# Optimization experiments

Measured on AMD Instinct MI355X. Metric: run time of the kernel, lower is better.

The kernel has to match this reference:

```python
import jax, jax.numpy as jnp
import numpy as np

N, E, C, H = 50000, 800000, 64, 64  # nodes, edges, channels, mlp hidden


def _seg_softmax(logits, seg, num_segments):
    # per-destination-node, per-channel softmax over incoming edges (PyG softmax)
    m = jax.ops.segment_max(logits, seg, num_segments=num_segments)
    m = jnp.where(jnp.isfinite(m), m, 0.0)
    e = jnp.exp(logits - m[seg])
    s = jax.ops.segment_sum(e, seg, num_segments=num_segments)
    return e / (s[seg] + 1e-16)


def setup_inputs() -> dict:
    key = jax.random.key(0)
    ks = jax.random.split(key, 16)

    def w(k, shape, fan_in):
        lim = 1.0 / np.sqrt(fan_in)
        return jax.random.uniform(k, shape, jnp.float32, -lim, lim)

    return dict(
        x=jax.random.normal(ks[0], (N, C), jnp.float32),
        pos=jax.random.uniform(ks[1], (N, 3), jnp.float32),
        edge_index=jax.random.randint(ks[2], (2, E), 0, N),
        # lin_in (Linear with bias)
        W_in=w(ks[3], (C, C), C), b_in=jnp.zeros((C,), jnp.float32),
        # PointTransformerConv internal linears (bias=False in PyG)
        W_lin=w(ks[4], (C, C), C),
        W_src=w(ks[5], (C, C), C),
        W_dst=w(ks[6], (C, C), C),
        # pos_nn: Linear(3,64) + ReLU + Linear(64,C)
        Wp1=w(ks[7], (3, H), 3), bp1=jnp.zeros((H,), jnp.float32),
        Wp2=w(ks[8], (H, C), H), bp2=jnp.zeros((C,), jnp.float32),
        # attn_nn: Linear(C,64) + ReLU + Linear(64,C)
        Wa1=w(ks[9], (C, H), C), ba1=jnp.zeros((H,), jnp.float32),
        Wa2=w(ks[10], (H, C), H), ba2=jnp.zeros((C,), jnp.float32),
        # lin_out
        W_out=w(ks[11], (C, C), C), b_out=jnp.zeros((C,), jnp.float32),
    )


def reference(x, pos, edge_index, W_in, b_in, W_lin, W_src, W_dst,
              Wp1, bp1, Wp2, bp2, Wa1, ba1, Wa2, ba2, W_out, b_out):
    n = x.shape[0]
    src, dst = edge_index[0], edge_index[1]
    # lin_in + ReLU
    h = jax.nn.relu(x @ W_in + b_in)                      # [N,C]
    # PointTransformerConv projections
    v = h @ W_lin                                         # values [N,C]
    a_src = h @ W_src                                     # alpha_j source term
    a_dst = h @ W_dst                                     # alpha_i dest term
    # per-edge positional encoding: pos_nn(pos_i - pos_j)
    rel = pos[dst] - pos[src]                             # [E,3]
    delta = jax.nn.relu(rel @ Wp1 + bp1) @ Wp2 + bp2      # [E,C]
    # attention logits: attn_nn(alpha_i - alpha_j + delta)
    alpha = a_dst[dst] - a_src[src] + delta               # [E,C]
    alpha = jax.nn.relu(alpha @ Wa1 + ba1) @ Wa2 + ba2    # [E,C]
    alpha = _seg_softmax(alpha, dst, n)
    # weighted scatter-sum aggregation: sum_j alpha * (x_j + delta)
    out = jax.ops.segment_sum(alpha * (v[src] + delta), dst, num_segments=n)
    # lin_out + ReLU
    return jax.nn.relu(out @ W_out + b_out)
```

## Files before the change

### kernel.cpp

```cpp
#include <hip/hip_runtime.h>

typedef unsigned short u16;
typedef unsigned int   u32;
typedef unsigned long long u64;
typedef __attribute__((ext_vector_type(8))) short bf16x8;
typedef __attribute__((ext_vector_type(4))) float f32x4;

#define DEV static __device__ __forceinline__

DEV u16 f2bf(float f){ union{float f; u32 i;} v; v.f=f; u32 u=v.i;
                       return (u16)((u + 0x7FFFu + ((u>>16)&1u))>>16); }
DEV float bf2f(u16 u){ union{u32 i; float f;} v; v.i=((u32)u)<<16; return v.f; }
DEV float bfl(u32 w){ return bf2f((u16)(w & 0xffffu)); }
DEV float bfh(u32 w){ return bf2f((u16)(w >> 16)); }
DEV u32 pk2(float a, float b){ return (u32)f2bf(a) | ((u32)f2bf(b) << 16); }
DEV void ldsfence(){ asm volatile("s_waitcnt lgkmcnt(0)" ::: "memory"); }

#define NBIAS 384
#define FB_P1 0
#define FB_P2 4
#define FB_A1 12
#define FB_A2 20
#define FB_IN 28
#define FB_LIN 36
#define FB_SRC 44
#define FB_DST 52
#define FB_OUT 60
#define NFRAG 68

#define LROW 70
#define LROWD 35

DEV bf16x8 fb_load(const u16* __restrict__ FB, int frag, int lane){
  union{ uint4 u; bf16x8 v; } w;
  w.u = *(const uint4*)(FB + ((size_t)(frag*64+lane))*8);
  return w.v;
}
DEV bf16x8 lds_read_chunk(const u32* l32, int dw){
  union{ u32 d[4]; bf16x8 v; } u;
#pragma unroll
  for(int p=0;p<4;p++) u.d[p] = l32[dw+p];
  return u.v;
}

__global__ __launch_bounds__(256) void k_prep(
  const float* __restrict__ Win, const float* __restrict__ Wlin,
  const float* __restrict__ Wsrc, const float* __restrict__ Wdst,
  const float* __restrict__ Wp1, const float* __restrict__ Wp2,
  const float* __restrict__ Wa1, const float* __restrict__ Wa2,
  const float* __restrict__ Wout,
  const float* __restrict__ bin, const float* __restrict__ bp1, const float* __restrict__ bp2,
  const float* __restrict__ ba1, const float* __restrict__ ba2, const float* __restrict__ bout,
  float* __restrict__ Bf, u16* __restrict__ FB)
{
  int idx = blockIdx.x*256 + threadIdx.x;
  if(idx < NBIAS){
    int which = idx >> 6, c = idx & 63;
    if(which == 3){
      float sacc = ba1[c];
      for(int k=0;k<64;k++) sacc += bp2[k]*Wa1[k*64+c];
      Bf[idx] = sacc;
    } else {
      const float* b;
      switch(which){ case 0:b=bin;break; case 1:b=bp1;break; case 2:b=bp2;break;
                     case 4:b=ba2;break; default:b=bout;break; }
      Bf[idx] = b[c];
    }
  } else if(idx < NBIAS + NFRAG*64){
    int j = idx - NBIAS;
    int frag = j >> 6, lane = j & 63;
    int t = lane & 15, q = lane >> 4;
    const float* src = nullptr; const float* fuse = nullptr;
    int K = 64, nt, s;
    if(frag < 4){ src = Wp1; K = 3; nt = frag; s = 0; }
    else if(frag < 12){ int g=frag-4;  src=Wp2;  nt=g>>1; s=g&1; }
    else if(frag < 20){ int g=frag-12; fuse=Wp2; nt=g>>1; s=g&1; }
    else if(frag < 28){ int g=frag-20; src=Wa2;  nt=g>>1; s=g&1; }
    else if(frag < 36){ int g=frag-28; src=Win;  nt=g>>1; s=g&1; }
    else if(frag < 44){ int g=frag-36; src=Wlin; nt=g>>1; s=g&1; }
    else if(frag < 52){ int g=frag-44; fuse=Wsrc; nt=g>>1; s=g&1; }
    else if(frag < 60){ int g=frag-52; fuse=Wdst; nt=g>>1; s=g&1; }
    else              { int g=frag-60; src=Wout; nt=g>>1; s=g&1; }
    u16* dst = FB + ((size_t)(frag*64+lane))*8;
    if(fuse){
      int col = nt*16 + t;
#pragma unroll
      for(int jj=0;jj<8;jj++){
        int k = s*32 + q*8 + jj;
        const float* ar = fuse + k*64;
        float accv = 0.f;
        for(int m=0;m<64;m++) accv += ar[m] * Wa1[m*64+col];
        dst[jj] = f2bf(accv);
      }
    } else {
#pragma unroll
      for(int jj=0;jj<8;jj++){
        int k = s*32 + q*8 + jj;
        dst[jj] = (k<K) ? f2bf(src[k*64 + nt*16 + t]) : (u16)0;
      }
    }
  }
}

__global__ __launch_bounds__(256) void k_node_m(
  const float* __restrict__ x, const float* __restrict__ Bf, const u16* __restrict__ FB,
  u16* __restrict__ vf, u16* __restrict__ asof, u16* __restrict__ adof,
  int N, int ntiles)
{
  __shared__ u16 sc16[4][16*LROW];
  int lane = threadIdx.x & 63, warp = threadIdx.x >> 6;
  int t = lane & 15, q = lane >> 4;
  int tile = blockIdx.x*4 + warp;
  if(tile >= ntiles) return;
  u16* lb = sc16[warp]; u32* lb32 = (u32*)lb;
  int r0 = tile*16;
  int row = r0 + t; if(row >= N) row = N-1;

  const float4* x4 = (const float4*)(x + (size_t)row*64);
  bf16x8 xa[2];
#pragma unroll
  for(int s=0;s<2;s++){
    float4 u0 = x4[s*8 + q*2], u1 = x4[s*8 + q*2 + 1];
    xa[s][0]=(short)f2bf(u0.x); xa[s][1]=(short)f2bf(u0.y);
    xa[s][2]=(short)f2bf(u0.z); xa[s][3]=(short)f2bf(u0.w);
    xa[s][4]=(short)f2bf(u1.x); xa[s][5]=(short)f2bf(u1.y);
    xa[s][6]=(short)f2bf(u1.z); xa[s][7]=(short)f2bf(u1.w);
  }
  f32x4 zero = {0.f,0.f,0.f,0.f};
  f32x4 acc[4];
#pragma unroll
  for(int nt=0;nt<4;nt++){
    acc[nt] = __builtin_amdgcn_mfma_f32_16x16x32_bf16(xa[0], fb_load(FB, FB_IN+nt*2+0, lane), zero, 0,0,0);
    acc[nt] = __builtin_amdgcn_mfma_f32_16x16x32_bf16(xa[1], fb_load(FB, FB_IN+nt*2+1, lane), acc[nt], 0,0,0);
  }
#pragma unroll
  for(int nt=0;nt<4;nt++)
#pragma unroll
    for(int r=0;r<4;r++)
      lb[(q*4+r)*LROW + nt*16 + t] = f2bf(fmaxf(acc[nt][r] + Bf[nt*16+t], 0.f));
  ldsfence();
  bf16x8 h0 = lds_read_chunk(lb32, t*LROWD + q*4);
  bf16x8 h1 = lds_read_chunk(lb32, t*LROWD + 16 + q*4);

  const int fb0[3] = {FB_LIN, FB_SRC, FB_DST};
  u16* Os[3] = {vf, asof, adof};
#pragma unroll
  for(int mtx=0; mtx<3; mtx++){
    f32x4 av[4];
#pragma unroll
    for(int nt=0;nt<4;nt++){
      av[nt] = __builtin_amdgcn_mfma_f32_16x16x32_bf16(h0, fb_load(FB, fb0[mtx]+nt*2+0, lane), zero, 0,0,0);
      av[nt] = __builtin_amdgcn_mfma_f32_16x16x32_bf16(h1, fb_load(FB, fb0[mtx]+nt*2+1, lane), av[nt], 0,0,0);
    }
    u16* O = Os[mtx];
#pragma unroll
    for(int r=0;r<4;r++){
      int rr = r0 + q*4 + r;
      if(rr < N){
        uint2 o;
        o.x = (u32)f2bf(av[0][r]) | ((u32)f2bf(av[1][r]) << 16);
        o.y = (u32)f2bf(av[2][r]) | ((u32)f2bf(av[3][r]) << 16);
        *(uint2*)(O + (size_t)rr*64 + t*4) = o;
      }
    }
  }
}

__global__ __launch_bounds__(256) void k_hist(const int* __restrict__ ei, int* __restrict__ deg, int E){
  int e = blockIdx.x*256 + threadIdx.x;
  if(e < E) atomicAdd(&deg[ei[(size_t)E + e]], 1);
}

__global__ __launch_bounds__(256) void k_scanA(const int* __restrict__ deg,
    int* __restrict__ row_start, int* __restrict__ bsum, int N){
  __shared__ int b[256];
  int tid = threadIdx.x, i = blockIdx.x*256 + tid;
  int v = (i<N) ? deg[i] : 0;
  b[tid] = v; __syncthreads();
#pragma unroll
  for(int off=1; off<256; off<<=1){
    int u = (tid>=off) ? b[tid-off] : 0;
    __syncthreads(); b[tid] += u; __syncthreads();
  }
  if(i<N) row_start[i] = b[tid] - v;
  if(tid==255) bsum[blockIdx.x] = b[255];
}
__global__ __launch_bounds__(256) void k_scanB(int* __restrict__ bsum,
    int* __restrict__ bsoff, int* __restrict__ row_start, int nb, int N){
  __shared__ int b[256];
  int tid = threadIdx.x;
  int v = (tid<nb) ? bsum[tid] : 0;
  b[tid] = v; __syncthreads();
#pragma unroll
  for(int off=1; off<256; off<<=1){
    int u = (tid>=off) ? b[tid-off] : 0;
    __syncthreads(); b[tid] += u; __syncthreads();
  }
  if(tid<nb) bsoff[tid] = b[tid] - v;
  if(tid==255) row_start[N] = b[255];
}
__global__ __launch_bounds__(256) void k_scanC(int* __restrict__ row_start,
    const int* __restrict__ bsoff, int N){
  int i = blockIdx.x*256 + threadIdx.x;
  if(i<N) row_start[i] += bsoff[blockIdx.x];
}

__global__ __launch_bounds__(256) void k_scatter(const int* __restrict__ ei,
    const int* __restrict__ row_start, int* __restrict__ cursor,
    int2* __restrict__ pair, int E){
  int e = blockIdx.x*256 + threadIdx.x;
  if(e >= E) return;
  int d = ei[(size_t)E + e];
  int p = atomicAdd(&cursor[d], 1);
  int2 pr; pr.x = ei[e]; pr.y = d;
  pair[row_start[d] + p] = pr;
}

DEV void flushseg(int d, float* numP, float* SP, const int* __restrict__ row_start,
                  float* __restrict__ num, float* __restrict__ S,
                  int lo, int hi, int q, int t){
  if(d < 0) return;
#pragma unroll
  for(int nt=0;nt<4;nt++){
    numP[nt] += __shfl_xor(numP[nt], 16, 64);
    numP[nt] += __shfl_xor(numP[nt], 32, 64);
    SP[nt]   += __shfl_xor(SP[nt],   16, 64);
    SP[nt]   += __shfl_xor(SP[nt],   32, 64);
  }
  bool partial = (row_start[d] < lo) || (row_start[d+1] > hi);
  if(q==0){
#pragma unroll
    for(int nt=0;nt<4;nt++){
      size_t off = (size_t)d*64 + nt*16 + t;
      if(partial){ atomicAdd(&num[off], numP[nt]); atomicAdd(&S[off], SP[nt]); }
      else       { num[off] = numP[nt]; S[off] = SP[nt]; }
    }
  }
#pragma unroll
  for(int nt=0;nt<4;nt++){ numP[nt]=0.f; SP[nt]=0.f; }
}

DEV void agg_tile(int tbase, int hi_w, int lo_w, int did,
                  const float wv[4][4], const float pd[4][4],
                  int& cur_d, float* numP, float* SP,
                  const int* __restrict__ row_start,
                  float* __restrict__ num, float* __restrict__ S, int q, int t){
  int m = 0;
  while(m < 16){
    int d0 = __shfl(did, m, 64);
    u32 same = (u32)(__ballot(did == d0) & 0xFFFFull);
    u32 rest = ~(same >> m);
    int len = __ffs(rest) - 1;
    int m1 = m + len;
    if(d0 != cur_d){
      flushseg(cur_d, numP, SP, row_start, num, S, lo_w, hi_w, q, t);
      cur_d = d0;
    }
#pragma unroll
    for(int r=0;r<4;r++){
      int mm = q*4 + r;
      bool use = (mm >= m) && (mm < m1) && ((tbase+mm) < hi_w);
      if(use){
#pragma unroll
        for(int nt=0;nt<4;nt++){
          numP[nt] += wv[nt][r] * pd[r][nt];
          SP[nt]   += wv[nt][r];
        }
      }
    }
    m = m1;
  }
}

__global__ __launch_bounds__(256,2) void k_edge_p4(
  const int* __restrict__ row_start, const int2* __restrict__ pair,
  const float* __restrict__ pos, const float* __restrict__ Bf, const u16* __restrict__ FB,
  const u16* __restrict__ vf, const u16* __restrict__ asof, const u16* __restrict__ adof,
  float* __restrict__ S, float* __restrict__ num, int E, int nsuper, int spw)
{
  __shared__ u16 sc16[4][2*32*LROW];
  int lane = threadIdx.x & 63, warp = threadIdx.x >> 6;
  int t = lane & 15, q = lane >> 4;
  int wid = blockIdx.x*4 + warp;
  int s0 = wid*spw, s1 = s0 + spw;
  if(s0 >= nsuper) return;
  if(s1 > nsuper) s1 = nsuper;
  int lo = s0*32, hi = s1*32; if(hi > E) hi = E;
  u16* lb = sc16[warp];             u32* lb32 = (u32*)lb;
  u16* lu = sc16[warp] + 32*LROW;   u32* lu32 = (u32*)lu;

  float bp1f[4], bp2f[4], baf[4], ba2f[4];
#pragma unroll
  for(int nt=0;nt<4;nt++){
    bp1f[nt]=Bf[ 64+nt*16+t]; bp2f[nt]=Bf[128+nt*16+t];
    baf[nt] =Bf[192+nt*16+t]; ba2f[nt]=Bf[256+nt*16+t];
  }
  const uint2* ad2 = (const uint2*)adof;
  const uint2* as2 = (const uint2*)asof;
  const uint2* v2  = (const uint2*)vf;
  f32x4 zero = {0.f,0.f,0.f,0.f};
  float numP[4] = {0,0,0,0}, SP[4] = {0,0,0,0};
  int cur_d = -1;

  for(int tb = lo; tb < hi; tb += 32){
    bool hasB = (tb+16) < hi;
    int ecA = tb + t;        if(ecA >= hi) ecA = hi-1;
    int ecB = tb + 16 + t;   if(ecB >= hi) ecB = hi-1;
    int2 spA = pair[ecA], spB = pair[ecB];
    int sidA = spA.x, didA = spA.y;
    int sidB = spB.x, didB = spB.y;
    int2 prA[4], prB[4];
#pragma unroll
    for(int r=0;r<4;r++){
      int eA = tb + q*4 + r;      if(eA >= hi) eA = hi-1;
      int eB = tb + 16 + q*4 + r; if(eB >= hi) eB = hi-1;
      prA[r] = pair[eA]; prB[r] = pair[eB];
    }

    bf16x8 a1A, a1B;
#pragma unroll
    for(int j=0;j<8;j++){ a1A[j]=0; a1B[j]=0; }
    if(q==0){
      a1A[0] = (short)f2bf(pos[(size_t)didA*3+0] - pos[(size_t)sidA*3+0]);
      a1A[1] = (short)f2bf(pos[(size_t)didA*3+1] - pos[(size_t)sidA*3+1]);
      a1A[2] = (short)f2bf(pos[(size_t)didA*3+2] - pos[(size_t)sidA*3+2]);
      a1B[0] = (short)f2bf(pos[(size_t)didB*3+0] - pos[(size_t)sidB*3+0]);
      a1B[1] = (short)f2bf(pos[(size_t)didB*3+1] - pos[(size_t)sidB*3+1]);
      a1B[2] = (short)f2bf(pos[(size_t)didB*3+2] - pos[(size_t)sidB*3+2]);
    }
    f32x4 accA[4], accB[4];
#pragma unroll
    for(int nt=0;nt<4;nt++){
      bf16x8 wp = fb_load(FB, FB_P1+nt, lane);
      accA[nt] = __builtin_amdgcn_mfma_f32_16x16x32_bf16(a1A, wp, zero, 0,0,0);
      accB[nt] = __builtin_amdgcn_mfma_f32_16x16x32_bf16(a1B, wp, zero, 0,0,0);
    }

#pragma unroll
    for(int nt=0;nt<4;nt++)
#pragma unroll
      for(int r=0;r<4;r++){
        lb[(     q*4+r)*LROW + nt*16 + t] = f2bf(fmaxf(accA[nt][r] + bp1f[nt], 0.f));
        lb[(16 + q*4+r)*LROW + nt*16 + t] = f2bf(fmaxf(accB[nt][r] + bp1f[nt], 0.f));
      }
    ldsfence();

    bf16x8 atA0 = lds_read_chunk(lb32, (t   )*LROWD + q*4);
    bf16x8 atA1 = lds_read_chunk(lb32, (t   )*LROWD + 16 + q*4);
    bf16x8 atB0 = lds_read_chunk(lb32, (t+16)*LROWD + q*4);
    bf16x8 atB1 = lds_read_chunk(lb32, (t+16)*LROWD + 16 + q*4);

    uint2 adwA[4], aswA[4], adwB[4], aswB[4];
#pragma unroll
    for(int r=0;r<4;r++){
      adwA[r] = ad2[(size_t)prA[r].y*16 + t];
      aswA[r] = as2[(size_t)prA[r].x*16 + t];
      adwB[r] = ad2[(size_t)prB[r].y*16 + t];
      aswB[r] = as2[(size_t)prB[r].x*16 + t];
    }

    u32 dpA[4][2], dpB[4][2];
#pragma unroll
    for(int nt=0;nt<4;nt++){
      bf16x8 w0 = fb_load(FB, FB_P2+nt*2+0, lane);
      bf16x8 w1 = fb_load(FB, FB_P2+nt*2+1, lane);
      f32x4 a = __builtin_amdgcn_mfma_f32_16x16x32_bf16(atA0, w0, zero, 0,0,0);
      a = __builtin_amdgcn_mfma_f32_16x16x32_bf16(atA1, w1, a, 0,0,0);
      f32x4 b = __builtin_amdgcn_mfma_f32_16x16x32_bf16(atB0, w0, zero, 0,0,0);
      b = __builtin_amdgcn_mfma_f32_16x16x32_bf16(atB1, w1, b, 0,0,0);
      dpA[nt][0] = pk2(a[0]+bp2f[nt], a[1]+bp2f[nt]);
      dpA[nt][1] = pk2(a[2]+bp2f[nt], a[3]+bp2f[nt]);
      dpB[nt][0] = pk2(b[0]+bp2f[nt], b[1]+bp2f[nt]);
      dpB[nt][1] = pk2(b[2]+bp2f[nt], b[3]+bp2f[nt]);
    }

#pragma unroll
    for(int nt=0;nt<4;nt++){
      bf16x8 w0 = fb_load(FB, FB_A1+nt*2+0, lane);
      bf16x8 w1 = fb_load(FB, FB_A1+nt*2+1, lane);
      f32x4 a = __builtin_amdgcn_mfma_f32_16x16x32_bf16(atA0, w0, zero, 0,0,0);
      a = __builtin_amdgcn_mfma_f32_16x16x32_bf16(atA1, w1, a, 0,0,0);
#pragma unroll
      for(int r=0;r<4;r++){
        u32 dw = (nt&2)? adwA[r].y : adwA[r].x;
        u32 sw = (nt&2)? aswA[r].y : aswA[r].x;
        float c = ((nt&1)? bfh(dw) : bfl(dw)) - ((nt&1)? bfh(sw) : bfl(sw));
        lu[(q*4+r)*LROW + nt*16 + t] = f2bf(fmaxf(a[r] + c + baf[nt], 0.f));
      }
    }
#pragma unroll
    for(int nt=0;nt<4;nt++){
      bf16x8 w0 = fb_load(FB, FB_A1+nt*2+0, lane);
      bf16x8 w1 = fb_load(FB, FB_A1+nt*2+1, lane);
      f32x4 b = __builtin_amdgcn_mfma_f32_16x16x32_bf16(atB0, w0, zero, 0,0,0);
      b = __builtin_amdgcn_mfma_f32_16x16x32_bf16(atB1, w1, b, 0,0,0);
#pragma unroll
      for(int r=0;r<4;r++){
        u32 dw = (nt&2)? adwB[r].y : adwB[r].x;
        u32 sw = (nt&2)? aswB[r].y : aswB[r].x;
        float c = ((nt&1)? bfh(dw) : bfl(dw)) - ((nt&1)? bfh(sw) : bfl(sw));
        lu[(16 + q*4+r)*LROW + nt*16 + t] = f2bf(fmaxf(b[r] + c + baf[nt], 0.f));
      }
    }

    uint2 vrawA[4], vrawB[4];
#pragma unroll
    for(int r=0;r<4;r++){
      vrawA[r] = v2[(size_t)prA[r].x*16 + t];
      vrawB[r] = v2[(size_t)prB[r].x*16 + t];
    }
    ldsfence();

    bf16x8 auA0 = lds_read_chunk(lu32, (t   )*LROWD + q*4);
    bf16x8 auA1 = lds_read_chunk(lu32, (t   )*LROWD + 16 + q*4);
    bf16x8 auB0 = lds_read_chunk(lu32, (t+16)*LROWD + q*4);
    bf16x8 auB1 = lds_read_chunk(lu32, (t+16)*LROWD + 16 + q*4);

    float wv[4][4], pd[4][4];
#pragma unroll
    for(int nt=0;nt<4;nt++){
      bf16x8 w0 = fb_load(FB, FB_A2+nt*2+0, lane);
      bf16x8 w1 = fb_load(FB, FB_A2+nt*2+1, lane);
      f32x4 a = __builtin_amdgcn_mfma_f32_16x16x32_bf16(auA0, w0, zero, 0,0,0);
      a = __builtin_amdgcn_mfma_f32_16x16x32_bf16(auA1, w1, a, 0,0,0);
#pragma unroll
      for(int r=0;r<4;r++)
        wv[nt][r] = ((tb + q*4 + r) < hi) ? __expf(fminf(a[r] + ba2f[nt], 80.f)) : 0.f;
    }
#pragma unroll
    for(int r=0;r<4;r++){
      float va[4] = { bfl(vrawA[r].x), bfh(vrawA[r].x), bfl(vrawA[r].y), bfh(vrawA[r].y) };
#pragma unroll
      for(int nt=0;nt<4;nt++){
        u32 dw = dpA[nt][r>>1];
        pd[r][nt] = va[nt] + ((r&1)? bfh(dw) : bfl(dw));
      }
    }
    agg_tile(tb, hi, lo, didA, wv, pd, cur_d, numP, SP, row_start, num, S, q, t);

    if(hasB){
#pragma unroll
      for(int nt=0;nt<4;nt++){
        bf16x8 w0 = fb_load(FB, FB_A2+nt*2+0, lane);
        bf16x8 w1 = fb_load(FB, FB_A2+nt*2+1, lane);
        f32x4 b = __builtin_amdgcn_mfma_f32_16x16x32_bf16(auB0, w0, zero, 0,0,0);
        b = __builtin_amdgcn_mfma_f32_16x16x32_bf16(auB1, w1, b, 0,0,0);
#pragma unroll
        for(int r=0;r<4;r++)
          wv[nt][r] = ((tb + 16 + q*4 + r) < hi) ? __expf(fminf(b[r] + ba2f[nt], 80.f)) : 0.f;
      }
#pragma unroll
      for(int r=0;r<4;r++){
        float vb[4] = { bfl(vrawB[r].x), bfh(vrawB[r].x), bfl(vrawB[r].y), bfh(vrawB[r].y) };
#pragma unroll
        for(int nt=0;nt<4;nt++){
          u32 dw = dpB[nt][r>>1];
          pd[r][nt] = vb[nt] + ((r&1)? bfh(dw) : bfl(dw));
        }
      }
      agg_tile(tb+16, hi, lo, didB, wv, pd, cur_d, numP, SP, row_start, num, S, q, t);
    }
  }
  flushseg(cur_d, numP, SP, row_start, num, S, lo, hi, q, t);
}

__global__ __launch_bounds__(256) void k_out_m(
  const float* __restrict__ num, const float* __restrict__ S,
  const float* __restrict__ Bf, const u16* __restrict__ FB,
  float* __restrict__ out, int N, int ntiles)
{
  int lane = threadIdx.x & 63, warp = threadIdx.x >> 6;
  int t = lane & 15, q = lane >> 4;
  int tile = blockIdx.x*4 + warp;
  if(tile >= ntiles) return;
  int r0 = tile*16;
  int row = r0 + t; if(row >= N) row = N-1;
  const float4* n4 = (const float4*)(num + (size_t)row*64);
  const float4* s4 = (const float4*)(S   + (size_t)row*64);
  bf16x8 af[2];
#pragma unroll
  for(int s=0;s<2;s++){
    float4 n0 = n4[s*8 + q*2], n1 = n4[s*8 + q*2 + 1];
    float4 s0 = s4[s*8 + q*2], s1 = s4[s*8 + q*2 + 1];
    af[s][0]=(short)f2bf(n0.x/(s0.x+1e-16f)); af[s][1]=(short)f2bf(n0.y/(s0.y+1e-16f));
    af[s][2]=(short)f2bf(n0.z/(s0.z+1e-16f)); af[s][3]=(short)f2bf(n0.w/(s0.w+1e-16f));
    af[s][4]=(short)f2bf(n1.x/(s1.x+1e-16f)); af[s][5]=(short)f2bf(n1.y/(s1.y+1e-16f));
    af[s][6]=(short)f2bf(n1.z/(s1.z+1e-16f)); af[s][7]=(short)f2bf(n1.w/(s1.w+1e-16f));
  }
  f32x4 zero = {0.f,0.f,0.f,0.f};
#pragma unroll
  for(int nt=0;nt<4;nt++){
    f32x4 a = __builtin_amdgcn_mfma_f32_16x16x32_bf16(af[0], fb_load(FB, FB_OUT+nt*2+0, lane), zero, 0,0,0);
    a = __builtin_amdgcn_mfma_f32_16x16x32_bf16(af[1], fb_load(FB, FB_OUT+nt*2+1, lane), a, 0,0,0);
    float b = Bf[320 + nt*16 + t];
#pragma unroll
    for(int r=0;r<4;r++){
      int rr = r0 + q*4 + r;
      if(rr < N) out[(size_t)rr*64 + nt*16 + t] = fmaxf(a[r] + b, 0.f);
    }
  }
}

extern "C" void kernel_launch(void* const* d_in, const int* in_sizes, int n_in,
                              void* d_out, int out_size, void* d_ws, size_t ws_size,
                              hipStream_t stream){
  const float* x   =(const float*)d_in[0];
  const float* pos =(const float*)d_in[1];
  const int*   ei  =(const int*)d_in[2];
  const float* Win =(const float*)d_in[3];  const float* bin=(const float*)d_in[4];
  const float* Wlin=(const float*)d_in[5];  const float* Wsrc=(const float*)d_in[6];
  const float* Wdst=(const float*)d_in[7];
  const float* Wp1 =(const float*)d_in[8];  const float* bp1=(const float*)d_in[9];
  const float* Wp2 =(const float*)d_in[10]; const float* bp2=(const float*)d_in[11];
  const float* Wa1 =(const float*)d_in[12]; const float* ba1=(const float*)d_in[13];
  const float* Wa2 =(const float*)d_in[14]; const float* ba2=(const float*)d_in[15];
  const float* Wout=(const float*)d_in[16]; const float* bout=(const float*)d_in[17];
  int N = in_sizes[0]/64;
  int E = in_sizes[2]/2;

  float* Bf    = (float*)d_ws;
  u16*   FB    = (u16*)(Bf + NBIAS);
  u16*   vfb   = FB + (size_t)NFRAG*64*8;
  u16*   asb   = vfb + (size_t)N*64;
  u16*   adb   = asb + (size_t)N*64;
  float* S     = (float*)(adb + (size_t)N*64);
  float* num   = S    + (size_t)N*64;
  int* deg       = (int*)(num + (size_t)N*64);
  int* cursor    = deg + N;
  int* row_start = cursor + N;
  int* bsum      = row_start + (N+1);
  int* bsoff     = bsum + 256;
  int2* pair     = (int2*)(bsoff + 256);

  int ntiles = (N+15)/16;
  int nsuper = (E+31)/32;
  int total_waves = 2048;
  int spw = (nsuper + total_waves - 1) / total_waves;
  int nwaves = (nsuper + spw - 1) / spw;
  int eblocks = (nwaves + 3) / 4;
  int nscb = (N+255)/256;

  hipMemsetAsync(deg, 0, (size_t)2*N*sizeof(int), stream);
  hipMemsetAsync(S, 0, (size_t)N*64*2*sizeof(float), stream);
  k_prep<<<dim3(19), dim3(256), 0, stream>>>(Win,Wlin,Wsrc,Wdst,Wp1,Wp2,Wa1,Wa2,Wout,
                                             bin,bp1,bp2,ba1,ba2,bout, Bf, FB);
  k_node_m<<<dim3((ntiles+3)/4), dim3(256), 0, stream>>>(x, Bf, FB, vfb, asb, adb, N, ntiles);
  k_hist<<<dim3((E+255)/256), dim3(256), 0, stream>>>(ei, deg, E);
  k_scanA<<<dim3(nscb), dim3(256), 0, stream>>>(deg, row_start, bsum, N);
  k_scanB<<<dim3(1),    dim3(256), 0, stream>>>(bsum, bsoff, row_start, nscb, N);
  k_scanC<<<dim3(nscb), dim3(256), 0, stream>>>(row_start, bsoff, N);
  k_scatter<<<dim3((E+255)/256), dim3(256), 0, stream>>>(ei, row_start, cursor, pair, E);
  k_edge_p4<<<dim3(eblocks), dim3(256), 0, stream>>>(row_start, pair, pos, Bf, FB,
                                                     vfb, asb, adb, S, num, E, nsuper, spw);
  k_out_m<<<dim3((ntiles+3)/4), dim3(256), 0, stream>>>(num, S, Bf, FB, (float*)d_out, N, ntiles);
}
```

Baseline: 359.0 us.

## Cut edge-kernel register pressure for higher occupancy and fold histogram into prep

The edge kernel no longer keeps the per-row edge pair arrays in registers. It re-reads pair entries at each use and loads the B-half values only inside the hasB branch, which allows launch bounds of 4 blocks per CU and double the wave count. The degree histogram is merged into the prep kernel as extra blocks, removing one launch. The trade is more redundant pair loads, which should mostly hit cache, in exchange for better latency hiding from higher occupancy.

```diff
diff --git a/kernel.cpp b/kernel.cpp
--- a/kernel.cpp
+++ b/kernel.cpp
@@ -43,6 +43,7 @@
   return u.v;
 }
 
+#define PREP_BLOCKS 19
 __global__ __launch_bounds__(256) void k_prep(
   const float* __restrict__ Win, const float* __restrict__ Wlin,
   const float* __restrict__ Wsrc, const float* __restrict__ Wdst,
@@ -51,8 +52,14 @@
   const float* __restrict__ Wout,
   const float* __restrict__ bin, const float* __restrict__ bp1, const float* __restrict__ bp2,
   const float* __restrict__ ba1, const float* __restrict__ ba2, const float* __restrict__ bout,
-  float* __restrict__ Bf, u16* __restrict__ FB)
+  float* __restrict__ Bf, u16* __restrict__ FB,
+  const int* __restrict__ ei, int* __restrict__ deg, int E)
 {
+  if(blockIdx.x >= PREP_BLOCKS){
+    int e = (blockIdx.x - PREP_BLOCKS)*256 + threadIdx.x;
+    if(e < E) atomicAdd(&deg[ei[(size_t)E + e]], 1);
+    return;
+  }
   int idx = blockIdx.x*256 + threadIdx.x;
   if(idx < NBIAS){
     int which = idx >> 6, c = idx & 63;
@@ -166,11 +173,6 @@
   }
 }
 
-__global__ __launch_bounds__(256) void k_hist(const int* __restrict__ ei, int* __restrict__ deg, int E){
-  int e = blockIdx.x*256 + threadIdx.x;
-  if(e < E) atomicAdd(&deg[ei[(size_t)E + e]], 1);
-}
-
 __global__ __launch_bounds__(256) void k_scanA(const int* __restrict__ deg,
     int* __restrict__ row_start, int* __restrict__ bsum, int N){
   __shared__ int b[256];
@@ -272,7 +274,7 @@
   }
 }
 
-__global__ __launch_bounds__(256,2) void k_edge_p4(
+__global__ __launch_bounds__(256,4) void k_edge_p5(
   const int* __restrict__ row_start, const int2* __restrict__ pair,
   const float* __restrict__ pos, const float* __restrict__ Bf, const u16* __restrict__ FB,
   const u16* __restrict__ vf, const u16* __restrict__ asof, const u16* __restrict__ adof,
@@ -309,13 +311,6 @@
     int2 spA = pair[ecA], spB = pair[ecB];
     int sidA = spA.x, didA = spA.y;
     int sidB = spB.x, didB = spB.y;
-    int2 prA[4], prB[4];
-#pragma unroll
-    for(int r=0;r<4;r++){
-      int eA = tb + q*4 + r;      if(eA >= hi) eA = hi-1;
-      int eB = tb + 16 + q*4 + r; if(eB >= hi) eB = hi-1;
-      prA[r] = pair[eA]; prB[r] = pair[eB];
-    }
 
     bf16x8 a1A, a1B;
 #pragma unroll
@@ -353,10 +348,13 @@
     uint2 adwA[4], aswA[4], adwB[4], aswB[4];
 #pragma unroll
     for(int r=0;r<4;r++){
-      adwA[r] = ad2[(size_t)prA[r].y*16 + t];
-      aswA[r] = as2[(size_t)prA[r].x*16 + t];
-      adwB[r] = ad2[(size_t)prB[r].y*16 + t];
-      aswB[r] = as2[(size_t)prB[r].x*16 + t];
+      int eA = tb + q*4 + r;      if(eA >= hi) eA = hi-1;
+      int eB = tb + 16 + q*4 + r; if(eB >= hi) eB = hi-1;
+      int2 pA = pair[eA], pB = pair[eB];
+      adwA[r] = ad2[(size_t)pA.y*16 + t];
+      aswA[r] = as2[(size_t)pA.x*16 + t];
+      adwB[r] = ad2[(size_t)pB.y*16 + t];
+      aswB[r] = as2[(size_t)pB.x*16 + t];
     }
 
     u32 dpA[4][2], dpB[4][2];
@@ -403,11 +401,11 @@
       }
     }
 
-    uint2 vrawA[4], vrawB[4];
+    uint2 vrawA[4];
 #pragma unroll
     for(int r=0;r<4;r++){
-      vrawA[r] = v2[(size_t)prA[r].x*16 + t];
-      vrawB[r] = v2[(size_t)prB[r].x*16 + t];
+      int eA = tb + q*4 + r; if(eA >= hi) eA = hi-1;
+      vrawA[r] = v2[(size_t)pair[eA].x*16 + t];
     }
     ldsfence();
 
@@ -439,6 +437,12 @@
     agg_tile(tb, hi, lo, didA, wv, pd, cur_d, numP, SP, row_start, num, S, q, t);
 
     if(hasB){
+      uint2 vrawB[4];
+#pragma unroll
+      for(int r=0;r<4;r++){
+        int eB = tb + 16 + q*4 + r; if(eB >= hi) eB = hi-1;
+        vrawB[r] = v2[(size_t)pair[eB].x*16 + t];
+      }
 #pragma unroll
       for(int nt=0;nt<4;nt++){
         bf16x8 w0 = fb_load(FB, FB_A2+nt*2+0, lane);
@@ -534,23 +538,24 @@
 
   int ntiles = (N+15)/16;
   int nsuper = (E+31)/32;
-  int total_waves = 2048;
+  int total_waves = 4096;
   int spw = (nsuper + total_waves - 1) / total_waves;
   int nwaves = (nsuper + spw - 1) / spw;
   int eblocks = (nwaves + 3) / 4;
   int nscb = (N+255)/256;
+  int hblocks = (E+255)/256;
 
   hipMemsetAsync(deg, 0, (size_t)2*N*sizeof(int), stream);
   hipMemsetAsync(S, 0, (size_t)N*64*2*sizeof(float), stream);
-  k_prep<<<dim3(19), dim3(256), 0, stream>>>(Win,Wlin,Wsrc,Wdst,Wp1,Wp2,Wa1,Wa2,Wout,
-                                             bin,bp1,bp2,ba1,ba2,bout, Bf, FB);
+  k_prep<<<dim3(PREP_BLOCKS + hblocks), dim3(256), 0, stream>>>(
+      Win,Wlin,Wsrc,Wdst,Wp1,Wp2,Wa1,Wa2,Wout,
+      bin,bp1,bp2,ba1,ba2,bout, Bf, FB, ei, deg, E);
   k_node_m<<<dim3((ntiles+3)/4), dim3(256), 0, stream>>>(x, Bf, FB, vfb, asb, adb, N, ntiles);
-  k_hist<<<dim3((E+255)/256), dim3(256), 0, stream>>>(ei, deg, E);
   k_scanA<<<dim3(nscb), dim3(256), 0, stream>>>(deg, row_start, bsum, N);
   k_scanB<<<dim3(1),    dim3(256), 0, stream>>>(bsum, bsoff, row_start, nscb, N);
   k_scanC<<<dim3(nscb), dim3(256), 0, stream>>>(row_start, bsoff, N);
   k_scatter<<<dim3((E+255)/256), dim3(256), 0, stream>>>(ei, row_start, cursor, pair, E);
-  k_edge_p4<<<dim3(eblocks), dim3(256), 0, stream>>>(row_start, pair, pos, Bf, FB,
+  k_edge_p5<<<dim3(eblocks), dim3(256), 0, stream>>>(row_start, pair, pos, Bf, FB,
                                                      vfb, asb, adb, S, num, E, nsuper, spw);
   k_out_m<<<dim3((ntiles+3)/4), dim3(256), 0, stream>>>(num, S, Bf, FB, (float*)d_out, N, ntiles);
 }
```

After: 535.0 us. +49.0%, slower.
